# Performance work log

Hardware: AMD Instinct MI355X
Metric: run time of the kernel (lower is better)

The kernel has to match this reference:

```python
import jax, jax.numpy as jnp
import numpy as np

VOCAB, EMB, HID, FF, NCLS = 1000, 32, 32, 16, 7
T, B = 512, 512


def setup_inputs() -> dict:
    key = jax.random.key(0)
    ks = jax.random.split(key, 10)
    s = 1.0 / np.sqrt(HID)
    return {
        "x": jax.random.randint(ks[0], (T, B), 0, VOCAB, dtype=jnp.int64)
        if jax.config.jax_enable_x64 else jax.random.randint(ks[0], (T, B), 0, VOCAB, dtype=jnp.int32),
        "emb": jax.random.normal(ks[1], (VOCAB, EMB), dtype=jnp.float32),
        "W_ih": jax.random.uniform(ks[2], (4 * HID, EMB), minval=-s, maxval=s, dtype=jnp.float32),
        "W_hh": jax.random.uniform(ks[3], (4 * HID, HID), minval=-s, maxval=s, dtype=jnp.float32),
        "b_ih": jax.random.uniform(ks[4], (4 * HID,), minval=-s, maxval=s, dtype=jnp.float32),
        "b_hh": jax.random.uniform(ks[5], (4 * HID,), minval=-s, maxval=s, dtype=jnp.float32),
        "W1": jax.random.uniform(ks[6], (FF, HID), minval=-s, maxval=s, dtype=jnp.float32),
        "b1": jax.random.uniform(ks[7], (FF,), minval=-s, maxval=s, dtype=jnp.float32),
        "W2": jax.random.uniform(ks[8], (NCLS, FF), minval=-s, maxval=s, dtype=jnp.float32),
        "b2": jax.random.uniform(ks[9], (NCLS,), minval=-s, maxval=s, dtype=jnp.float32),
    }


def _lstm(xg, W_hh):
    # xg: (T, B, 4H) precomputed input-to-gate projections (incl. both biases)
    Bn = xg.shape[1]
    h0 = jnp.zeros((Bn, HID), xg.dtype)
    c0 = jnp.zeros((Bn, HID), xg.dtype)

    def step(carry, xg_t):
        h, c = carry
        g = xg_t + h @ W_hh.T  # (B, 4H)
        i, f, gg, o = jnp.split(g, 4, axis=-1)  # PyTorch gate order i,f,g,o
        i = jax.nn.sigmoid(i)
        f = jax.nn.sigmoid(f)
        gg = jnp.tanh(gg)
        o = jax.nn.sigmoid(o)
        c = f * c + i * gg
        h = o * jnp.tanh(c)
        return (h, c), h

    _, hs = jax.lax.scan(step, (h0, c0), xg)
    return hs  # (T, B, H)


def reference(x, emb, W_ih, W_hh, b_ih, b_hh, W1, b1, W2, b2):
    e = emb[x]  # (T, B, EMB) embedding lookup
    xg = jnp.einsum('tbe,ge->tbg', e, W_ih) + b_ih + b_hh  # (T, B, 4H)
    hs = _lstm(xg, W_hh)  # (T, B, H)
    z = jax.nn.relu(jnp.einsum('tbh,fh->tbf', hs, W1) + b1)  # (T, B, FF)
    logits = jnp.einsum('tbf,cf->tbc', z, W2) + b2  # (T, B, NCLS)
    # torch F.softmax with dim=None on a 3D tensor softmaxes over dim 0
    return jax.nn.softmax(logits, axis=0)
```

## Files before the change

### kernel.cpp

```cpp
#include <hip/hip_runtime.h>
#include <math.h>

#define TT    512
#define BB    512
#define HID   32
#define EMB   32
#define FFD   16
#define NCLS  7
#define VOCABN 1000

typedef float v2f __attribute__((ext_vector_type(2)));
typedef float v4f __attribute__((ext_vector_type(4)));

#define NLOG2E  (-1.4426950408889634f)
#define N2LOG2E (-2.8853900817779268f)

__device__ __forceinline__ float rl(float v, int k) {
    return __int_as_float(__builtin_amdgcn_readlane(__float_as_int(v), k));
}
__device__ __forceinline__ float fast_rcp(float x) {
#if defined(__has_builtin)
#if __has_builtin(__builtin_amdgcn_rcpf)
    return __builtin_amdgcn_rcpf(x);
#else
    return 1.0f / x;
#endif
#else
    return 1.0f / x;
#endif
}
__device__ __forceinline__ float sigf(float x) { return fast_rcp(1.0f + __expf(-x)); }
__device__ __forceinline__ float tanh_fast(float x) { return 2.0f * sigf(2.0f * x) - 1.0f; }

__device__ __forceinline__ v2f fma2(v2f a, v2f b, v2f c) {
#if defined(__has_builtin)
#if __has_builtin(__builtin_elementwise_fma)
    return __builtin_elementwise_fma(a, b, c);
#else
    v2f r; r.x = fmaf(a.x, b.x, c.x); r.y = fmaf(a.y, b.y, c.y); return r;
#endif
#else
    v2f r; r.x = fmaf(a.x, b.x, c.x); r.y = fmaf(a.y, b.y, c.y); return r;
#endif
}

__device__ __forceinline__ float xhalf_swap(float v) {
#if defined(__has_builtin)
#if __has_builtin(__builtin_amdgcn_permlane32_swap)
    const unsigned u = __float_as_uint(v);
    auto r = __builtin_amdgcn_permlane32_swap(u, u, false, false);
    return __uint_as_float((r[0] ^ r[1]) ^ u);
#else
    return __shfl_xor(v, 32);
#endif
#else
    return __shfl_xor(v, 32);
#endif
}

__global__ __launch_bounds__(64) void build_xg(
    const float* __restrict__ emb, const float* __restrict__ W_ih,
    const float* __restrict__ b_ih, const float* __restrict__ b_hh,
    float2* __restrict__ tab, int scaled)
{
    const int v = blockIdx.x;
    const int j = threadIdx.x;
    const float* e  = emb + v * EMB;
    const float* w0 = W_ih + j * EMB;
    const float* w1 = W_ih + (j + 64) * EMB;
    float a0 = b_ih[j]      + b_hh[j];
    float a1 = b_ih[j + 64] + b_hh[j + 64];
    #pragma unroll
    for (int k = 0; k < EMB; ++k) {
        const float ek = e[k];
        a0 = fmaf(w0[k], ek, a0);
        a1 = fmaf(w1[k], ek, a1);
    }
    float s0 = 1.0f, s1 = 1.0f;
    if (scaled) { s0 = NLOG2E; s1 = (j < 32) ? N2LOG2E : NLOG2E; }
    tab[v * 64 + j] = make_float2(a0 * s0, a1 * s1);
}

__global__ __launch_bounds__(64)
__attribute__((amdgpu_waves_per_eu(1, 1)))
void lstm_rec(
    const int* __restrict__ x, const float2* __restrict__ tab,
    const float* __restrict__ W_hh, float* __restrict__ hsout)
{
    const int b  = blockIdx.x;
    const int j  = threadIdx.x;
    const int m  = j & 31;
    const bool lo = j < 32;

    __shared__ __align__(16) float sh[8 * HID];

    const float fA = NLOG2E;
    const float fB = lo ? N2LOG2E : NLOG2E;
    const v2f sA2 = {fA, fA};
    const v2f sB2 = {fB, fB};
    const v4f* WA = (const v4f*)(W_hh + j * HID);
    const v4f* WB = (const v4f*)(W_hh + (j + 64) * HID);
    v4f t;
    v2f wpa0,wpa1,wpa2,wpa3,wpa4,wpa5,wpa6,wpa7,wpa8,wpa9,wpa10,wpa11,wpa12,wpa13,wpa14,wpa15;
    v2f wpb0,wpb1,wpb2,wpb3,wpb4,wpb5,wpb6,wpb7,wpb8,wpb9,wpb10,wpb11,wpb12,wpb13,wpb14,wpb15;
    t = WA[0]; wpa0  = t.lo * sA2; wpa1  = t.hi * sA2;
    t = WA[1]; wpa2  = t.lo * sA2; wpa3  = t.hi * sA2;
    t = WA[2]; wpa4  = t.lo * sA2; wpa5  = t.hi * sA2;
    t = WA[3]; wpa6  = t.lo * sA2; wpa7  = t.hi * sA2;
    t = WA[4]; wpa8  = t.lo * sA2; wpa9  = t.hi * sA2;
    t = WA[5]; wpa10 = t.lo * sA2; wpa11 = t.hi * sA2;
    t = WA[6]; wpa12 = t.lo * sA2; wpa13 = t.hi * sA2;
    t = WA[7]; wpa14 = t.lo * sA2; wpa15 = t.hi * sA2;
    t = WB[0]; wpb0  = t.lo * sB2; wpb1  = t.hi * sB2;
    t = WB[1]; wpb2  = t.lo * sB2; wpb3  = t.hi * sB2;
    t = WB[2]; wpb4  = t.lo * sB2; wpb5  = t.hi * sB2;
    t = WB[3]; wpb6  = t.lo * sB2; wpb7  = t.hi * sB2;
    t = WB[4]; wpb8  = t.lo * sB2; wpb9  = t.hi * sB2;
    t = WB[5]; wpb10 = t.lo * sB2; wpb11 = t.hi * sB2;
    t = WB[6]; wpb12 = t.lo * sB2; wpb13 = t.hi * sB2;
    t = WB[7]; wpb14 = t.lo * sB2; wpb15 = t.hi * sB2;

    float h = 0.f, c = 0.f;
    float* hrow0 = hsout + (size_t)b * TT * HID;

    if (lo) sh[7 * HID + m] = 0.0f;

    int xiB[8];
    float2 cxg[8];
    {
        int xi0[8];
        #pragma unroll
        for (int u = 0; u < 8; ++u) xi0[u] = x[u * BB + b];
        #pragma unroll
        for (int u = 0; u < 8; ++u) xiB[u] = x[(8 + u) * BB + b];
        #pragma unroll
        for (int u = 0; u < 8; ++u) cxg[u] = tab[(size_t)xi0[u] * 64 + j];
    }

    for (int t8 = 0; t8 < TT / 8; ++t8) {
        float2 nxg[8];
        #pragma unroll
        for (int u = 0; u < 8; ++u) nxg[u] = tab[(size_t)xiB[u] * 64 + j];
        int xiN[8];
        const int nb2 = (t8 + 2 < TT / 8) ? (t8 + 2) * 8 : 0;
        #pragma unroll
        for (int u = 0; u < 8; ++u) xiN[u] = x[(nb2 + u) * BB + b];

        #pragma unroll
        for (int u = 0; u < 8; ++u) {
            const float* hb = sh + ((u + 7) & 7) * HID;
            const v4f h0 = *(const v4f*)(hb + 0);
            const v4f h1 = *(const v4f*)(hb + 4);
            const v4f h2 = *(const v4f*)(hb + 8);
            const v4f h3 = *(const v4f*)(hb + 12);
            const v4f h4 = *(const v4f*)(hb + 16);
            const v4f h5 = *(const v4f*)(hb + 20);
            const v4f h6 = *(const v4f*)(hb + 24);
            const v4f h7 = *(const v4f*)(hb + 28);

            v2f aP0 = {cxg[u].x, 0.f}, aP1 = {0.f, 0.f};
            v2f aQ0 = {cxg[u].y, 0.f}, aQ1 = {0.f, 0.f};
            aP0 = fma2(wpa0,  h0.lo, aP0);  aP1 = fma2(wpa1,  h0.hi, aP1);
            aQ0 = fma2(wpb0,  h0.lo, aQ0);  aQ1 = fma2(wpb1,  h0.hi, aQ1);
            aP0 = fma2(wpa2,  h1.lo, aP0);  aP1 = fma2(wpa3,  h1.hi, aP1);
            aQ0 = fma2(wpb2,  h1.lo, aQ0);  aQ1 = fma2(wpb3,  h1.hi, aQ1);
            aP0 = fma2(wpa4,  h2.lo, aP0);  aP1 = fma2(wpa5,  h2.hi, aP1);
            aQ0 = fma2(wpb4,  h2.lo, aQ0);  aQ1 = fma2(wpb5,  h2.hi, aQ1);
            aP0 = fma2(wpa6,  h3.lo, aP0);  aP1 = fma2(wpa7,  h3.hi, aP1);
            aQ0 = fma2(wpb6,  h3.lo, aQ0);  aQ1 = fma2(wpb7,  h3.hi, aQ1);
            aP0 = fma2(wpa8,  h4.lo, aP0);  aP1 = fma2(wpa9,  h4.hi, aP1);
            aQ0 = fma2(wpb8,  h4.lo, aQ0);  aQ1 = fma2(wpb9,  h4.hi, aQ1);
            aP0 = fma2(wpa10, h5.lo, aP0);  aP1 = fma2(wpa11, h5.hi, aP1);
            aQ0 = fma2(wpb10, h5.lo, aQ0);  aQ1 = fma2(wpb11, h5.hi, aQ1);
            aP0 = fma2(wpa12, h6.lo, aP0);  aP1 = fma2(wpa13, h6.hi, aP1);
            aQ0 = fma2(wpb12, h6.lo, aQ0);  aQ1 = fma2(wpb13, h6.hi, aQ1);
            aP0 = fma2(wpa14, h7.lo, aP0);  aP1 = fma2(wpa15, h7.hi, aP1);
            aQ0 = fma2(wpb14, h7.lo, aQ0);  aQ1 = fma2(wpb15, h7.hi, aQ1);
            const v2f aP = aP0 + aP1;
            const v2f aQ = aQ0 + aQ1;
            const float accA = aP.x + aP.y;
            const float accB = aQ.x + aQ.y;

            const float actA = fast_rcp(1.0f + __builtin_exp2f(accA));
            const float sgB  = fast_rcp(1.0f + __builtin_exp2f(accB));
            const float actB = lo ? fmaf(2.0f, sgB, -1.0f) : sgB;
            const float oA = xhalf_swap(actA);
            const float oB = xhalf_swap(actB);
            const float gi = lo ? actA : oA;
            const float gf = lo ? oA   : actA;
            const float gg = lo ? actB : oB;
            const float go = lo ? oB   : actB;
            c = fmaf(gf, c, gi * gg);
            const float tc = fmaf(2.0f,
                fast_rcp(1.0f + __builtin_exp2f(c * N2LOG2E)), -1.0f);
            h = go * tc;

            if (lo) sh[u * HID + m] = h;
        }
        const float4 v = *(const float4*)(sh + j * 4);
        *(float4*)(hrow0 + t8 * 8 * HID + j * 4) = v;

        #pragma unroll
        for (int u = 0; u < 8; ++u) { cxg[u] = nxg[u]; xiB[u] = xiN[u]; }
    }
}

__global__ __launch_bounds__(256) void ff_softmax(
    const float* __restrict__ hs,
    const float* __restrict__ W1, const float* __restrict__ b1,
    const float* __restrict__ W2, const float* __restrict__ b2,
    float* __restrict__ out)
{
    const int b    = blockIdx.x;
    const int tid  = threadIdx.x;
    const int lane = tid & 63, wv = tid >> 6;
    const int t0   = tid * 2;

    __shared__ float redM[4][NCLS];
    __shared__ float redS[4][NCLS];

    float4 hv[16];
    const float4* hb = (const float4*)(hs + ((size_t)b * TT + t0) * HID);
    #pragma unroll
    for (int q = 0; q < 16; ++q) hv[q] = hb[q];

    float lg[2][NCLS];
    #pragma unroll
    for (int r = 0; r < 2; ++r) {
        const float* hr = (const float*)(hv + 8 * r);
        float z[FFD];
        #pragma unroll
        for (int f = 0; f < FFD; ++f) {
            float a = b1[f];
            #pragma unroll
            for (int k = 0; k < HID; ++k) a = fmaf(W1[f * HID + k], hr[k], a);
            z[f] = fmaxf(a, 0.f);
        }
        #pragma unroll
        for (int cc = 0; cc < NCLS; ++cc) {
            float a = b2[cc];
            #pragma unroll
            for (int f = 0; f < FFD; ++f) a = fmaf(W2[cc * FFD + f], z[f], a);
            lg[r][cc] = a;
        }
    }

    float M[NCLS], S[NCLS];
    #pragma unroll
    for (int cc = 0; cc < NCLS; ++cc) {
        float mm = fmaxf(lg[0][cc], lg[1][cc]);
        #pragma unroll
        for (int off = 32; off; off >>= 1) mm = fmaxf(mm, __shfl_xor(mm, off));
        if (lane == 0) redM[wv][cc] = mm;
    }
    __syncthreads();
    #pragma unroll
    for (int cc = 0; cc < NCLS; ++cc)
        M[cc] = fmaxf(fmaxf(redM[0][cc], redM[1][cc]), fmaxf(redM[2][cc], redM[3][cc]));

    #pragma unroll
    for (int cc = 0; cc < NCLS; ++cc) {
        float ss = __expf(lg[0][cc] - M[cc]) + __expf(lg[1][cc] - M[cc]);
        #pragma unroll
        for (int off = 32; off; off >>= 1) ss += __shfl_xor(ss, off);
        if (lane == 0) redS[wv][cc] = ss;
    }
    __syncthreads();
    #pragma unroll
    for (int cc = 0; cc < NCLS; ++cc)
        S[cc] = (redS[0][cc] + redS[1][cc]) + (redS[2][cc] + redS[3][cc]);

    #pragma unroll
    for (int r = 0; r < 2; ++r) {
        float* o = out + ((size_t)(t0 + r) * BB + b) * NCLS;
        #pragma unroll
        for (int cc = 0; cc < NCLS; ++cc)
            o[cc] = __expf(lg[r][cc] - M[cc]) * fast_rcp(S[cc]);
    }
}

template <bool TAB>
__global__ __launch_bounds__(64) void lstm_all(
    const int* __restrict__ x, const float* __restrict__ emb,
    const float* __restrict__ W_ih, const float* __restrict__ W_hh,
    const float* __restrict__ b_ih, const float* __restrict__ b_hh,
    const float* __restrict__ W1, const float* __restrict__ b1,
    const float* __restrict__ W2, const float* __restrict__ b2,
    const float2* __restrict__ tab, float* __restrict__ out)
{
    const int b  = blockIdx.x;
    const int j  = threadIdx.x;
    const int m  = j & 31;
    const bool lo = j < 32;
    const int rA = j, rB = j + 64;

    float whhA[HID], whhB[HID];
    #pragma unroll
    for (int k = 0; k < HID; k += 4) {
        float4 a;
        a = *(const float4*)(W_hh + rA * HID + k); whhA[k]=a.x; whhA[k+1]=a.y; whhA[k+2]=a.z; whhA[k+3]=a.w;
        a = *(const float4*)(W_hh + rB * HID + k); whhB[k]=a.x; whhB[k+1]=a.y; whhB[k+2]=a.z; whhB[k+3]=a.w;
    }
    float wihA[HID], wihB[HID];
    float biasA = 0.f, biasB = 0.f;
    if constexpr (!TAB) {
        #pragma unroll
        for (int k = 0; k < HID; k += 4) {
            float4 a;
            a = *(const float4*)(W_ih + rA * HID + k); wihA[k]=a.x; wihA[k+1]=a.y; wihA[k+2]=a.z; wihA[k+3]=a.w;
            a = *(const float4*)(W_ih + rB * HID + k); wihB[k]=a.x; wihB[k+1]=a.y; wihB[k+2]=a.z; wihB[k+3]=a.w;
        }
        biasA = b_ih[rA] + b_hh[rA];
        biasB = b_ih[rB] + b_hh[rB];
    }
    const int f16 = j & 15;
    float w1r[HID];
    #pragma unroll
    for (int k = 0; k < HID; ++k) w1r[k] = W1[f16 * HID + k];
    const int cls = j & 7;
    const int c7  = (cls < NCLS) ? cls : 0;
    float w2r[FFD];
    #pragma unroll
    for (int f = 0; f < FFD; ++f) w2r[f] = W2[c7 * FFD + f];
    const float b1v = b1[f16];
    const float b2v = b2[c7];

    float h = 0.f, c = 0.f;
    float mrun = -3.0e38f, srun = 0.f;

    auto gates = [&](float accA, float accB) {
        const float actA = sigf(accA);
        const float sB   = lo ? 2.0f * accB : accB;
        const float sgB  = sigf(sB);
        const float actB = lo ? 2.0f * sgB - 1.0f : sgB;
        const float oA = __shfl_xor(actA, 32);
        const float oB = __shfl_xor(actB, 32);
        const float gi = lo ? actA : oA;
        const float gf = lo ? oA   : actA;
        const float gg = lo ? actB : oB;
        const float go = lo ? oB   : actB;
        c = fmaf(gf, c, gi * gg);
        h = go * tanh_fast(c);
    };

    auto ff_head = [&](int t_out, const float* hsv) {
        float z0 = b1v, z1 = 0.f;
        #pragma unroll
        for (int k = 0; k < HID; k += 2) {
            z0 = fmaf(w1r[k],     hsv[k],     z0);
            z1 = fmaf(w1r[k + 1], hsv[k + 1], z1);
        }
        const float z = fmaxf(z0 + z1, 0.0f);
        float lgv = b2v;
        #pragma unroll
        for (int f = 0; f < FFD; ++f) lgv = fmaf(w2r[f], rl(z, f), lgv);
        const float mn = fmaxf(mrun, lgv);
        srun = fmaf(srun, __expf(mrun - mn), __expf(lgv - mn));
        mrun = mn;
        if (j < NCLS) out[(t_out * BB + b) * NCLS + j] = lgv;
    };

    int xvn1 = x[1 * BB + b];
    int xvn2 = x[2 * BB + b];
    float2 xg = make_float2(0.f, 0.f);
    float eA = 0.f;
    if constexpr (TAB) xg = tab[(size_t)x[b] * 64 + j];
    else               eA = emb[x[b] * EMB + m];

    if constexpr (TAB) {
        gates(xg.x, xg.y);
    } else {
        float es[EMB];
        #pragma unroll
        for (int k = 0; k < EMB; ++k) es[k] = rl(eA, k);
        float p0 = biasA, p1 = 0.f, q0 = biasB, q1 = 0.f;
        #pragma unroll
        for (int k = 0; k < EMB; k += 2) {
            p0 = fmaf(wihA[k],   es[k],   p0); p1 = fmaf(wihA[k+1], es[k+1], p1);
            q0 = fmaf(wihB[k],   es[k],   q0); q1 = fmaf(wihB[k+1], es[k+1], q1);
        }
        gates(p0 + p1, q0 + q1);
    }
    if constexpr (TAB) xg = tab[(size_t)xvn1 * 64 + j];
    else               eA = emb[xvn1 * EMB + m];
    xvn1 = xvn2;
    xvn2 = x[3 * BB + b];

    for (int t = 1; t < TT; ++t) {
        float2 xg_n = make_float2(0.f, 0.f);
        float  e_n  = 0.f;
        if (t + 1 < TT) {
            if constexpr (TAB) xg_n = tab[(size_t)xvn1 * 64 + j];
            else               e_n  = emb[xvn1 * EMB + m];
        }
        const int xv_n3 = (t + 3 < TT) ? x[(t + 3) * BB + b] : 0;

        float hsv[HID];
        #pragma unroll
        for (int k = 0; k < HID; ++k) hsv[k] = rl(h, k);

        ff_head(t - 1, hsv);

        float p0, p1 = 0.f, q0, q1 = 0.f;
        if constexpr (TAB) { p0 = xg.x; q0 = xg.y; }
        else               { p0 = biasA; q0 = biasB; }
        if constexpr (!TAB) {
            float es[EMB];
            #pragma unroll
            for (int k = 0; k < EMB; ++k) es[k] = rl(eA, k);
            #pragma unroll
            for (int k = 0; k < EMB; k += 2) {
                p0 = fmaf(wihA[k],   es[k],   p0); p1 = fmaf(wihA[k+1], es[k+1], p1);
                q0 = fmaf(wihB[k],   es[k],   q0); q1 = fmaf(wihB[k+1], es[k+1], q1);
            }
        }
        #pragma unroll
        for (int k = 0; k < HID; k += 2) {
            p0 = fmaf(whhA[k],   hsv[k],   p0); p1 = fmaf(whhA[k+1], hsv[k+1], p1);
            q0 = fmaf(whhB[k],   hsv[k],   q0); q1 = fmaf(whhB[k+1], hsv[k+1], q1);
        }
        gates(p0 + p1, q0 + q1);

        xg = xg_n; eA = e_n; xvn1 = xvn2; xvn2 = xv_n3;
    }

    {
        float hsv[HID];
        #pragma unroll
        for (int k = 0; k < HID; ++k) hsv[k] = rl(h, k);
        ff_head(TT - 1, hsv);
    }

    #pragma unroll 1
    for (int cc = 0; cc < NCLS; ++cc) {
        const float mc = rl(mrun, cc);
        const float sc = rl(srun, cc);
        const float ic = 1.0f / sc;
        #pragma unroll
        for (int i = 0; i < TT / 64; ++i) {
            const int t = j + 64 * i;
            const int a = (t * BB + b) * NCLS + cc;
            out[a] = __expf(out[a] - mc) * ic;
        }
    }
}

extern "C" void kernel_launch(void* const* d_in, const int* in_sizes, int n_in,
                              void* d_out, int out_size, void* d_ws, size_t ws_size,
                              hipStream_t stream) {
    const int*   x   = (const int*)  d_in[0];
    const float* emb = (const float*)d_in[1];
    const float* Wih = (const float*)d_in[2];
    const float* Whh = (const float*)d_in[3];
    const float* bih = (const float*)d_in[4];
    const float* bhh = (const float*)d_in[5];
    const float* W1  = (const float*)d_in[6];
    const float* b1  = (const float*)d_in[7];
    const float* W2  = (const float*)d_in[8];
    const float* b2  = (const float*)d_in[9];
    float* out = (float*)d_out;

    const size_t tab_bytes = (size_t)VOCABN * 128 * sizeof(float);
    const size_t hs_off    = 524288;
    const size_t hs_bytes  = (size_t)BB * TT * HID * sizeof(float);
    if (ws_size >= hs_off + hs_bytes) {
        float2* tab = (float2*)d_ws;
        float*  hs  = (float*)((char*)d_ws + hs_off);
        build_xg<<<VOCABN, 64, 0, stream>>>(emb, Wih, bih, bhh, tab, 1);
        lstm_rec<<<BB, 64, 0, stream>>>(x, tab, Whh, hs);
        ff_softmax<<<BB, 256, 0, stream>>>(hs, W1, b1, W2, b2, out);
    } else if (ws_size >= tab_bytes) {
        float2* tab = (float2*)d_ws;
        build_xg<<<VOCABN, 64, 0, stream>>>(emb, Wih, bih, bhh, tab, 0);
        lstm_all<true><<<BB, 64, 0, stream>>>(x, emb, Wih, Whh, bih, bhh,
                                              W1, b1, W2, b2, tab, out);
    } else {
        lstm_all<false><<<BB, 64, 0, stream>>>(x, emb, Wih, Whh, bih, bhh,
                                               W1, b1, W2, b2, nullptr, out);
    }
}
```

Before: 240.1 us.

## Interleave two batch sequences per wavefront in LSTM recurrence

Each 64-thread block now runs the recurrence for two independent batch elements, alternating their timesteps, and launches half as many blocks. The aim is to hide the serial dependency latency (LDS reads, transcendental ops, lane swaps) of one sequence behind the other's independent work. In exchange it uses more registers and halves the block count from 512 to 256. On a 256-CU device this leaves roughly one wave per CU, so per-CU serial work doubles unless the interleaving hides latency well.

```diff
diff --git a/kernel.cpp b/kernel.cpp
--- a/kernel.cpp
+++ b/kernel.cpp
@@ -83,16 +83,18 @@
 
 __global__ __launch_bounds__(64)
 __attribute__((amdgpu_waves_per_eu(1, 1)))
-void lstm_rec(
+void lstm_rec2(
     const int* __restrict__ x, const float2* __restrict__ tab,
     const float* __restrict__ W_hh, float* __restrict__ hsout)
 {
-    const int b  = blockIdx.x;
+    const int b0 = blockIdx.x * 2;
+    const int b1 = b0 + 1;
     const int j  = threadIdx.x;
     const int m  = j & 31;
     const bool lo = j < 32;
 
-    __shared__ __align__(16) float sh[8 * HID];
+    __shared__ __align__(16) float sh0[8 * HID];
+    __shared__ __align__(16) float sh1[8 * HID];
 
     const float fA = NLOG2E;
     const float fB = lo ? N2LOG2E : NLOG2E;
@@ -120,88 +122,110 @@
     t = WB[6]; wpb12 = t.lo * sB2; wpb13 = t.hi * sB2;
     t = WB[7]; wpb14 = t.lo * sB2; wpb15 = t.hi * sB2;
 
-    float h = 0.f, c = 0.f;
-    float* hrow0 = hsout + (size_t)b * TT * HID;
-
-    if (lo) sh[7 * HID + m] = 0.0f;
-
-    int xiB[8];
-    float2 cxg[8];
+    float c0 = 0.f, c1 = 0.f;
+    float* hrow0 = hsout + (size_t)b0 * TT * HID;
+    float* hrow1 = hsout + (size_t)b1 * TT * HID;
+
+    sh0[7 * HID + m] = 0.0f;
+    sh1[7 * HID + m] = 0.0f;
+
+    auto dostep = [&](int u, float* shc, const float2 xgv, float& cc) {
+        const float* hb = shc + ((u + 7) & 7) * HID;
+        const v4f h0 = *(const v4f*)(hb + 0);
+        const v4f h1 = *(const v4f*)(hb + 4);
+        const v4f h2 = *(const v4f*)(hb + 8);
+        const v4f h3 = *(const v4f*)(hb + 12);
+        const v4f h4 = *(const v4f*)(hb + 16);
+        const v4f h5 = *(const v4f*)(hb + 20);
+        const v4f h6 = *(const v4f*)(hb + 24);
+        const v4f h7 = *(const v4f*)(hb + 28);
+
+        v2f aP0 = {xgv.x, 0.f}, aP1 = {0.f, 0.f};
+        v2f aQ0 = {xgv.y, 0.f}, aQ1 = {0.f, 0.f};
+        aP0 = fma2(wpa0,  h0.lo, aP0);  aP1 = fma2(wpa1,  h0.hi, aP1);
+        aQ0 = fma2(wpb0,  h0.lo, aQ0);  aQ1 = fma2(wpb1,  h0.hi, aQ1);
+        aP0 = fma2(wpa2,  h1.lo, aP0);  aP1 = fma2(wpa3,  h1.hi, aP1);
+        aQ0 = fma2(wpb2,  h1.lo, aQ0);  aQ1 = fma2(wpb3,  h1.hi, aQ1);
+        aP0 = fma2(wpa4,  h2.lo, aP0);  aP1 = fma2(wpa5,  h2.hi, aP1);
+        aQ0 = fma2(wpb4,  h2.lo, aQ0);  aQ1 = fma2(wpb5,  h2.hi, aQ1);
+        aP0 = fma2(wpa6,  h3.lo, aP0);  aP1 = fma2(wpa7,  h3.hi, aP1);
+        aQ0 = fma2(wpb6,  h3.lo, aQ0);  aQ1 = fma2(wpb7,  h3.hi, aQ1);
+        aP0 = fma2(wpa8,  h4.lo, aP0);  aP1 = fma2(wpa9,  h4.hi, aP1);
+        aQ0 = fma2(wpb8,  h4.lo, aQ0);  aQ1 = fma2(wpb9,  h4.hi, aQ1);
+        aP0 = fma2(wpa10, h5.lo, aP0);  aP1 = fma2(wpa11, h5.hi, aP1);
+        aQ0 = fma2(wpb10, h5.lo, aQ0);  aQ1 = fma2(wpb11, h5.hi, aQ1);
+        aP0 = fma2(wpa12, h6.lo, aP0);  aP1 = fma2(wpa13, h6.hi, aP1);
+        aQ0 = fma2(wpb12, h6.lo, aQ0);  aQ1 = fma2(wpb13, h6.hi, aQ1);
+        aP0 = fma2(wpa14, h7.lo, aP0);  aP1 = fma2(wpa15, h7.hi, aP1);
+        aQ0 = fma2(wpb14, h7.lo, aQ0);  aQ1 = fma2(wpb15, h7.hi, aQ1);
+        const v2f aP = aP0 + aP1;
+        const v2f aQ = aQ0 + aQ1;
+        const float accA = aP.x + aP.y;
+        const float accB = aQ.x + aQ.y;
+
+        const float actA = fast_rcp(1.0f + __builtin_exp2f(accA));
+        const float sgB  = fast_rcp(1.0f + __builtin_exp2f(accB));
+        const float actB = lo ? fmaf(2.0f, sgB, -1.0f) : sgB;
+        const float oA = xhalf_swap(actA);
+        const float oB = xhalf_swap(actB);
+        const float gi = lo ? actA : oA;
+        const float gf = lo ? oA   : actA;
+        const float gg = lo ? actB : oB;
+        const float go = lo ? oB   : actB;
+        cc = fmaf(gf, cc, gi * gg);
+        const float tc = fmaf(2.0f,
+            fast_rcp(1.0f + __builtin_exp2f(cc * N2LOG2E)), -1.0f);
+        const float hv = go * tc;
+
+        shc[u * HID + m] = hv;
+    };
+
+    int xiB0[8], xiB1[8];
+    float2 cxg0[8], cxg1[8];
     {
-        int xi0[8];
-        #pragma unroll
-        for (int u = 0; u < 8; ++u) xi0[u] = x[u * BB + b];
-        #pragma unroll
-        for (int u = 0; u < 8; ++u) xiB[u] = x[(8 + u) * BB + b];
-        #pragma unroll
-        for (int u = 0; u < 8; ++u) cxg[u] = tab[(size_t)xi0[u] * 64 + j];
+        int xi00[8], xi01[8];
+        #pragma unroll
+        for (int u = 0; u < 8; ++u) { xi00[u] = x[u * BB + b0]; xi01[u] = x[u * BB + b1]; }
+        #pragma unroll
+        for (int u = 0; u < 8; ++u) { xiB0[u] = x[(8 + u) * BB + b0]; xiB1[u] = x[(8 + u) * BB + b1]; }
+        #pragma unroll
+        for (int u = 0; u < 8; ++u) {
+            cxg0[u] = tab[(size_t)xi00[u] * 64 + j];
+            cxg1[u] = tab[(size_t)xi01[u] * 64 + j];
+        }
     }
 
     for (int t8 = 0; t8 < TT / 8; ++t8) {
-        float2 nxg[8];
-        #pragma unroll
-        for (int u = 0; u < 8; ++u) nxg[u] = tab[(size_t)xiB[u] * 64 + j];
-        int xiN[8];
+        float2 nxg0[8], nxg1[8];
+        #pragma unroll
+        for (int u = 0; u < 8; ++u) {
+            nxg0[u] = tab[(size_t)xiB0[u] * 64 + j];
+            nxg1[u] = tab[(size_t)xiB1[u] * 64 + j];
+        }
+        int xiN0[8], xiN1[8];
         const int nb2 = (t8 + 2 < TT / 8) ? (t8 + 2) * 8 : 0;
         #pragma unroll
-        for (int u = 0; u < 8; ++u) xiN[u] = x[(nb2 + u) * BB + b];
-
-        #pragma unroll
         for (int u = 0; u < 8; ++u) {
-            const float* hb = sh + ((u + 7) & 7) * HID;
-            const v4f h0 = *(const v4f*)(hb + 0);
-            const v4f h1 = *(const v4f*)(hb + 4);
-            const v4f h2 = *(const v4f*)(hb + 8);
-            const v4f h3 = *(const v4f*)(hb + 12);
-            const v4f h4 = *(const v4f*)(hb + 16);
-            const v4f h5 = *(const v4f*)(hb + 20);
-            const v4f h6 = *(const v4f*)(hb + 24);
-            const v4f h7 = *(const v4f*)(hb + 28);
-
-            v2f aP0 = {cxg[u].x, 0.f}, aP1 = {0.f, 0.f};
-            v2f aQ0 = {cxg[u].y, 0.f}, aQ1 = {0.f, 0.f};
-            aP0 = fma2(wpa0,  h0.lo, aP0);  aP1 = fma2(wpa1,  h0.hi, aP1);
-            aQ0 = fma2(wpb0,  h0.lo, aQ0);  aQ1 = fma2(wpb1,  h0.hi, aQ1);
-            aP0 = fma2(wpa2,  h1.lo, aP0);  aP1 = fma2(wpa3,  h1.hi, aP1);
-            aQ0 = fma2(wpb2,  h1.lo, aQ0);  aQ1 = fma2(wpb3,  h1.hi, aQ1);
-            aP0 = fma2(wpa4,  h2.lo, aP0);  aP1 = fma2(wpa5,  h2.hi, aP1);
-            aQ0 = fma2(wpb4,  h2.lo, aQ0);  aQ1 = fma2(wpb5,  h2.hi, aQ1);
-            aP0 = fma2(wpa6,  h3.lo, aP0);  aP1 = fma2(wpa7,  h3.hi, aP1);
-            aQ0 = fma2(wpb6,  h3.lo, aQ0);  aQ1 = fma2(wpb7,  h3.hi, aQ1);
-            aP0 = fma2(wpa8,  h4.lo, aP0);  aP1 = fma2(wpa9,  h4.hi, aP1);
-            aQ0 = fma2(wpb8,  h4.lo, aQ0);  aQ1 = fma2(wpb9,  h4.hi, aQ1);
-            aP0 = fma2(wpa10, h5.lo, aP0);  aP1 = fma2(wpa11, h5.hi, aP1);
-            aQ0 = fma2(wpb10, h5.lo, aQ0);  aQ1 = fma2(wpb11, h5.hi, aQ1);
-            aP0 = fma2(wpa12, h6.lo, aP0);  aP1 = fma2(wpa13, h6.hi, aP1);
-            aQ0 = fma2(wpb12, h6.lo, aQ0);  aQ1 = fma2(wpb13, h6.hi, aQ1);
-            aP0 = fma2(wpa14, h7.lo, aP0);  aP1 = fma2(wpa15, h7.hi, aP1);
-            aQ0 = fma2(wpb14, h7.lo, aQ0);  aQ1 = fma2(wpb15, h7.hi, aQ1);
-            const v2f aP = aP0 + aP1;
-            const v2f aQ = aQ0 + aQ1;
-            const float accA = aP.x + aP.y;
-            const float accB = aQ.x + aQ.y;
-
-            const float actA = fast_rcp(1.0f + __builtin_exp2f(accA));
-            const float sgB  = fast_rcp(1.0f + __builtin_exp2f(accB));
-            const float actB = lo ? fmaf(2.0f, sgB, -1.0f) : sgB;
-            const float oA = xhalf_swap(actA);
-            const float oB = xhalf_swap(actB);
-            const float gi = lo ? actA : oA;
-            const float gf = lo ? oA   : actA;
-            const float gg = lo ? actB : oB;
-            const float go = lo ? oB   : actB;
-            c = fmaf(gf, c, gi * gg);
-            const float tc = fmaf(2.0f,
-                fast_rcp(1.0f + __builtin_exp2f(c * N2LOG2E)), -1.0f);
-            h = go * tc;
-
-            if (lo) sh[u * HID + m] = h;
-        }
-        const float4 v = *(const float4*)(sh + j * 4);
-        *(float4*)(hrow0 + t8 * 8 * HID + j * 4) = v;
-
-        #pragma unroll
-        for (int u = 0; u < 8; ++u) { cxg[u] = nxg[u]; xiB[u] = xiN[u]; }
+            xiN0[u] = x[(nb2 + u) * BB + b0];
+            xiN1[u] = x[(nb2 + u) * BB + b1];
+        }
+
+        #pragma unroll
+        for (int u = 0; u < 8; ++u) {
+            dostep(u, sh0, cxg0[u], c0);
+            dostep(u, sh1, cxg1[u], c1);
+        }
+
+        const float4 v0 = *(const float4*)(sh0 + j * 4);
+        *(float4*)(hrow0 + t8 * 8 * HID + j * 4) = v0;
+        const float4 v1 = *(const float4*)(sh1 + j * 4);
+        *(float4*)(hrow1 + t8 * 8 * HID + j * 4) = v1;
+
+        #pragma unroll
+        for (int u = 0; u < 8; ++u) {
+            cxg0[u] = nxg0[u]; xiB0[u] = xiN0[u];
+            cxg1[u] = nxg1[u]; xiB1[u] = xiN1[u];
+        }
     }
 }
 
@@ -467,7 +491,7 @@
         float2* tab = (float2*)d_ws;
         float*  hs  = (float*)((char*)d_ws + hs_off);
         build_xg<<<VOCABN, 64, 0, stream>>>(emb, Wih, bih, bhh, tab, 1);
-        lstm_rec<<<BB, 64, 0, stream>>>(x, tab, Whh, hs);
+        lstm_rec2<<<BB / 2, 64, 0, stream>>>(x, tab, Whh, hs);
         ff_softmax<<<BB, 256, 0, stream>>>(hs, W1, b1, W2, b2, out);
     } else if (ws_size >= tab_bytes) {
         float2* tab = (float2*)d_ws;
```

New measurement: 358.2 us. 49.2% more time.

## Broadcast hidden state via lane swizzles/DPP instead of LDS round-trip

Applied to the files above, without the earlier changes.

Removes the shared-memory buffer used to broadcast h each timestep. Each lane instead gathers all 32 h values through ds_swizzle and DPP xor permutations, and the W_hh weights are loaded in a matching permuted order so each lane's dot product stays correct. The h output is now written straight to global memory per step instead of being staged and stored as float4. This targets the LDS write/read latency on the serial recurrence path, at the cost of many cross-lane ops and narrower, duplicated global stores.

```diff
diff --git a/kernel.cpp b/kernel.cpp
--- a/kernel.cpp
+++ b/kernel.cpp
@@ -57,6 +57,20 @@
     return __shfl_xor(v, 32);
 #endif
 }
+
+#define SWZF(x, imm) __int_as_float(__builtin_amdgcn_ds_swizzle(__float_as_int(x), (imm)))
+#if defined(__has_builtin)
+#if __has_builtin(__builtin_amdgcn_mov_dpp)
+#define XOR1F(x) __int_as_float(__builtin_amdgcn_mov_dpp(__float_as_int(x), 0xB1, 0xF, 0xF, true))
+#define XOR2F(x) __int_as_float(__builtin_amdgcn_mov_dpp(__float_as_int(x), 0x4E, 0xF, 0xF, true))
+#else
+#define XOR1F(x) SWZF(x, 0x041F)
+#define XOR2F(x) SWZF(x, 0x081F)
+#endif
+#else
+#define XOR1F(x) SWZF(x, 0x041F)
+#define XOR2F(x) SWZF(x, 0x081F)
+#endif
 
 __global__ __launch_bounds__(64) void build_xg(
     const float* __restrict__ emb, const float* __restrict__ W_ih,
@@ -92,38 +106,25 @@
     const int m  = j & 31;
     const bool lo = j < 32;
 
-    __shared__ __align__(16) float sh[8 * HID];
-
     const float fA = NLOG2E;
     const float fB = lo ? N2LOG2E : NLOG2E;
     const v2f sA2 = {fA, fA};
     const v2f sB2 = {fB, fB};
-    const v4f* WA = (const v4f*)(W_hh + j * HID);
-    const v4f* WB = (const v4f*)(W_hh + (j + 64) * HID);
-    v4f t;
+    const float* WrA = W_hh + (size_t)j * HID;
+    const float* WrB = W_hh + (size_t)(j + 64) * HID;
     v2f wpa0,wpa1,wpa2,wpa3,wpa4,wpa5,wpa6,wpa7,wpa8,wpa9,wpa10,wpa11,wpa12,wpa13,wpa14,wpa15;
     v2f wpb0,wpb1,wpb2,wpb3,wpb4,wpb5,wpb6,wpb7,wpb8,wpb9,wpb10,wpb11,wpb12,wpb13,wpb14,wpb15;
-    t = WA[0]; wpa0  = t.lo * sA2; wpa1  = t.hi * sA2;
-    t = WA[1]; wpa2  = t.lo * sA2; wpa3  = t.hi * sA2;
-    t = WA[2]; wpa4  = t.lo * sA2; wpa5  = t.hi * sA2;
-    t = WA[3]; wpa6  = t.lo * sA2; wpa7  = t.hi * sA2;
-    t = WA[4]; wpa8  = t.lo * sA2; wpa9  = t.hi * sA2;
-    t = WA[5]; wpa10 = t.lo * sA2; wpa11 = t.hi * sA2;
-    t = WA[6]; wpa12 = t.lo * sA2; wpa13 = t.hi * sA2;
-    t = WA[7]; wpa14 = t.lo * sA2; wpa15 = t.hi * sA2;
-    t = WB[0]; wpb0  = t.lo * sB2; wpb1  = t.hi * sB2;
-    t = WB[1]; wpb2  = t.lo * sB2; wpb3  = t.hi * sB2;
-    t = WB[2]; wpb4  = t.lo * sB2; wpb5  = t.hi * sB2;
-    t = WB[3]; wpb6  = t.lo * sB2; wpb7  = t.hi * sB2;
-    t = WB[4]; wpb8  = t.lo * sB2; wpb9  = t.hi * sB2;
-    t = WB[5]; wpb10 = t.lo * sB2; wpb11 = t.hi * sB2;
-    t = WB[6]; wpb12 = t.lo * sB2; wpb13 = t.hi * sB2;
-    t = WB[7]; wpb14 = t.lo * sB2; wpb15 = t.hi * sB2;
+    #define LDW(t, s0, s1) \
+        wpa##t = (v2f){WrA[m ^ (s0)], WrA[m ^ (s1)]} * sA2; \
+        wpb##t = (v2f){WrB[m ^ (s0)], WrB[m ^ (s1)]} * sB2;
+    LDW(0,  0,  4)  LDW(1,  8, 12)  LDW(2, 16, 20)  LDW(3, 24, 28)
+    LDW(4,  1,  5)  LDW(5,  9, 13)  LDW(6, 17, 21)  LDW(7, 25, 29)
+    LDW(8,  2,  6)  LDW(9, 10, 14)  LDW(10,18, 22)  LDW(11,26, 30)
+    LDW(12, 3,  7)  LDW(13,11, 15)  LDW(14,19, 23)  LDW(15,27, 31)
+    #undef LDW
 
     float h = 0.f, c = 0.f;
     float* hrow0 = hsout + (size_t)b * TT * HID;
-
-    if (lo) sh[7 * HID + m] = 0.0f;
 
     int xiB[8];
     float2 cxg[8];
@@ -148,34 +149,53 @@
 
         #pragma unroll
         for (int u = 0; u < 8; ++u) {
-            const float* hb = sh + ((u + 7) & 7) * HID;
-            const v4f h0 = *(const v4f*)(hb + 0);
-            const v4f h1 = *(const v4f*)(hb + 4);
-            const v4f h2 = *(const v4f*)(hb + 8);
-            const v4f h3 = *(const v4f*)(hb + 12);
-            const v4f h4 = *(const v4f*)(hb + 16);
-            const v4f h5 = *(const v4f*)(hb + 20);
-            const v4f h6 = *(const v4f*)(hb + 24);
-            const v4f h7 = *(const v4f*)(hb + 28);
+            const float u0 = h;
+            const float u1 = SWZF(u0, 0x101F);
+            const float u2 = SWZF(u0, 0x201F);
+            const float u3 = SWZF(u1, 0x201F);
+            const float u4 = SWZF(u0, 0x401F);
+            const float u5 = SWZF(u1, 0x401F);
+            const float u6 = SWZF(u2, 0x401F);
+            const float u7 = SWZF(u3, 0x401F);
+            const float u8  = XOR1F(u0),  u9  = XOR1F(u1);
+            const float u10 = XOR1F(u2),  u11 = XOR1F(u3);
+            const float u12 = XOR1F(u4),  u13 = XOR1F(u5);
+            const float u14 = XOR1F(u6),  u15 = XOR1F(u7);
+            const float u16 = XOR2F(u0),  u17 = XOR2F(u1);
+            const float u18 = XOR2F(u2),  u19 = XOR2F(u3);
+            const float u20 = XOR2F(u4),  u21 = XOR2F(u5);
+            const float u22 = XOR2F(u6),  u23 = XOR2F(u7);
+            const float u24 = XOR2F(u8),  u25 = XOR2F(u9);
+            const float u26 = XOR2F(u10), u27 = XOR2F(u11);
+            const float u28 = XOR2F(u12), u29 = XOR2F(u13);
+            const float u30 = XOR2F(u14), u31 = XOR2F(u15);
+            const v2f hp0  = {u0,  u1},  hp1  = {u2,  u3};
+            const v2f hp2  = {u4,  u5},  hp3  = {u6,  u7};
+            const v2f hp4  = {u8,  u9},  hp5  = {u10, u11};
+            const v2f hp6  = {u12, u13}, hp7  = {u14, u15};
+            const v2f hp8  = {u16, u17}, hp9  = {u18, u19};
+            const v2f hp10 = {u20, u21}, hp11 = {u22, u23};
+            const v2f hp12 = {u24, u25}, hp13 = {u26, u27};
+            const v2f hp14 = {u28, u29}, hp15 = {u30, u31};
 
             v2f aP0 = {cxg[u].x, 0.f}, aP1 = {0.f, 0.f};
             v2f aQ0 = {cxg[u].y, 0.f}, aQ1 = {0.f, 0.f};
-            aP0 = fma2(wpa0,  h0.lo, aP0);  aP1 = fma2(wpa1,  h0.hi, aP1);
-            aQ0 = fma2(wpb0,  h0.lo, aQ0);  aQ1 = fma2(wpb1,  h0.hi, aQ1);
-            aP0 = fma2(wpa2,  h1.lo, aP0);  aP1 = fma2(wpa3,  h1.hi, aP1);
-            aQ0 = fma2(wpb2,  h1.lo, aQ0);  aQ1 = fma2(wpb3,  h1.hi, aQ1);
-            aP0 = fma2(wpa4,  h2.lo, aP0);  aP1 = fma2(wpa5,  h2.hi, aP1);
-            aQ0 = fma2(wpb4,  h2.lo, aQ0);  aQ1 = fma2(wpb5,  h2.hi, aQ1);
-            aP0 = fma2(wpa6,  h3.lo, aP0);  aP1 = fma2(wpa7,  h3.hi, aP1);
-            aQ0 = fma2(wpb6,  h3.lo, aQ0);  aQ1 = fma2(wpb7,  h3.hi, aQ1);
-            aP0 = fma2(wpa8,  h4.lo, aP0);  aP1 = fma2(wpa9,  h4.hi, aP1);
-            aQ0 = fma2(wpb8,  h4.lo, aQ0);  aQ1 = fma2(wpb9,  h4.hi, aQ1);
-            aP0 = fma2(wpa10, h5.lo, aP0);  aP1 = fma2(wpa11, h5.hi, aP1);
-            aQ0 = fma2(wpb10, h5.lo, aQ0);  aQ1 = fma2(wpb11, h5.hi, aQ1);
-            aP0 = fma2(wpa12, h6.lo, aP0);  aP1 = fma2(wpa13, h6.hi, aP1);
-            aQ0 = fma2(wpb12, h6.lo, aQ0);  aQ1 = fma2(wpb13, h6.hi, aQ1);
-            aP0 = fma2(wpa14, h7.lo, aP0);  aP1 = fma2(wpa15, h7.hi, aP1);
-            aQ0 = fma2(wpb14, h7.lo, aQ0);  aQ1 = fma2(wpb15, h7.hi, aQ1);
+            aP0 = fma2(wpa0,  hp0,  aP0);  aQ0 = fma2(wpb0,  hp0,  aQ0);
+            aP1 = fma2(wpa4,  hp4,  aP1);  aQ1 = fma2(wpb4,  hp4,  aQ1);
+            aP0 = fma2(wpa8,  hp8,  aP0);  aQ0 = fma2(wpb8,  hp8,  aQ0);
+            aP1 = fma2(wpa12, hp12, aP1);  aQ1 = fma2(wpb12, hp12, aQ1);
+            aP0 = fma2(wpa1,  hp1,  aP0);  aQ0 = fma2(wpb1,  hp1,  aQ0);
+            aP1 = fma2(wpa2,  hp2,  aP1);  aQ1 = fma2(wpb2,  hp2,  aQ1);
+            aP0 = fma2(wpa5,  hp5,  aP0);  aQ0 = fma2(wpb5,  hp5,  aQ0);
+            aP1 = fma2(wpa6,  hp6,  aP1);  aQ1 = fma2(wpb6,  hp6,  aQ1);
+            aP0 = fma2(wpa9,  hp9,  aP0);  aQ0 = fma2(wpb9,  hp9,  aQ0);
+            aP1 = fma2(wpa10, hp10, aP1);  aQ1 = fma2(wpb10, hp10, aQ1);
+            aP0 = fma2(wpa13, hp13, aP0);  aQ0 = fma2(wpb13, hp13, aQ0);
+            aP1 = fma2(wpa14, hp14, aP1);  aQ1 = fma2(wpb14, hp14, aQ1);
+            aP0 = fma2(wpa3,  hp3,  aP0);  aQ0 = fma2(wpb3,  hp3,  aQ0);
+            aP1 = fma2(wpa7,  hp7,  aP1);  aQ1 = fma2(wpb7,  hp7,  aQ1);
+            aP0 = fma2(wpa11, hp11, aP0);  aQ0 = fma2(wpb11, hp11, aQ0);
+            aP1 = fma2(wpa15, hp15, aP1);  aQ1 = fma2(wpb15, hp15, aQ1);
             const v2f aP = aP0 + aP1;
             const v2f aQ = aQ0 + aQ1;
             const float accA = aP.x + aP.y;
@@ -195,10 +215,8 @@
                 fast_rcp(1.0f + __builtin_exp2f(c * N2LOG2E)), -1.0f);
             h = go * tc;
 
-            if (lo) sh[u * HID + m] = h;
-        }
-        const float4 v = *(const float4*)(sh + j * 4);
-        *(float4*)(hrow0 + t8 * 8 * HID + j * 4) = v;
+            hrow0[(t8 * 8 + u) * HID + m] = h;
+        }
 
         #pragma unroll
         for (int u = 0; u < 8; ++u) { cxg[u] = nxg[u]; xiB[u] = xiN[u]; }
```

After: 287.3 us. +19.7%, slower.

## Fuse feed-forward head and online softmax into the LSTM recurrence kernel

Applied to the files above, without the earlier changes.

Removes the separate ff_softmax kernel and the hidden-state buffer. Each recurrence step now computes the FF head from the previous timestep's h, which is already in registers or LDS, writes raw logits, and keeps a per-class online max and sum for the softmax. A final pass rescales the logits in place. This drops the global round trip of the hidden states but adds per-step work to the latency-bound recurrence critical path.

```diff
diff --git a/kernel.cpp b/kernel.cpp
--- a/kernel.cpp
+++ b/kernel.cpp
@@ -83,9 +83,12 @@
 
 __global__ __launch_bounds__(64)
 __attribute__((amdgpu_waves_per_eu(1, 1)))
-void lstm_rec(
+void lstm_fused(
     const int* __restrict__ x, const float2* __restrict__ tab,
-    const float* __restrict__ W_hh, float* __restrict__ hsout)
+    const float* __restrict__ W_hh,
+    const float* __restrict__ W1, const float* __restrict__ b1,
+    const float* __restrict__ W2, const float* __restrict__ b2,
+    float* __restrict__ out)
 {
     const int b  = blockIdx.x;
     const int j  = threadIdx.x;
@@ -120,8 +123,52 @@
     t = WB[6]; wpb12 = t.lo * sB2; wpb13 = t.hi * sB2;
     t = WB[7]; wpb14 = t.lo * sB2; wpb15 = t.hi * sB2;
 
+    const int f16 = j & 15;
+    const int cls = j & 7;
+    const int c7  = (cls < NCLS) ? cls : 0;
+    v2f w1p0,w1p1,w1p2,w1p3,w1p4,w1p5,w1p6,w1p7,w1p8,w1p9,w1p10,w1p11,w1p12,w1p13,w1p14,w1p15;
+    {
+        const v4f* W1r = (const v4f*)(W1 + f16 * HID);
+        v4f q;
+        q = W1r[0]; w1p0  = q.lo; w1p1  = q.hi;
+        q = W1r[1]; w1p2  = q.lo; w1p3  = q.hi;
+        q = W1r[2]; w1p4  = q.lo; w1p5  = q.hi;
+        q = W1r[3]; w1p6  = q.lo; w1p7  = q.hi;
+        q = W1r[4]; w1p8  = q.lo; w1p9  = q.hi;
+        q = W1r[5]; w1p10 = q.lo; w1p11 = q.hi;
+        q = W1r[6]; w1p12 = q.lo; w1p13 = q.hi;
+        q = W1r[7]; w1p14 = q.lo; w1p15 = q.hi;
+    }
+    float w2r[FFD];
+    #pragma unroll
+    for (int f = 0; f < FFD; ++f) w2r[f] = W2[c7 * FFD + f];
+    const float b1v = b1[f16];
+    const float b2v = b2[c7];
+
     float h = 0.f, c = 0.f;
-    float* hrow0 = hsout + (size_t)b * TT * HID;
+    float mrun = -3.0e38f, srun = 0.f;
+
+    auto ff_head = [&](int t_out, v4f h0, v4f h1, v4f h2, v4f h3,
+                                  v4f h4, v4f h5, v4f h6, v4f h7) {
+        v2f z0 = {b1v, 0.f}, z1 = {0.f, 0.f};
+        z0 = fma2(w1p0,  h0.lo, z0);  z1 = fma2(w1p1,  h0.hi, z1);
+        z0 = fma2(w1p2,  h1.lo, z0);  z1 = fma2(w1p3,  h1.hi, z1);
+        z0 = fma2(w1p4,  h2.lo, z0);  z1 = fma2(w1p5,  h2.hi, z1);
+        z0 = fma2(w1p6,  h3.lo, z0);  z1 = fma2(w1p7,  h3.hi, z1);
+        z0 = fma2(w1p8,  h4.lo, z0);  z1 = fma2(w1p9,  h4.hi, z1);
+        z0 = fma2(w1p10, h5.lo, z0);  z1 = fma2(w1p11, h5.hi, z1);
+        z0 = fma2(w1p12, h6.lo, z0);  z1 = fma2(w1p13, h6.hi, z1);
+        z0 = fma2(w1p14, h7.lo, z0);  z1 = fma2(w1p15, h7.hi, z1);
+        const v2f zs = z0 + z1;
+        const float z = fmaxf(zs.x + zs.y, 0.0f);
+        float lgv = b2v;
+        #pragma unroll
+        for (int f = 0; f < FFD; ++f) lgv = fmaf(w2r[f], rl(z, f), lgv);
+        const float mn = fmaxf(mrun, lgv);
+        srun = fmaf(srun, __expf(mrun - mn), __expf(lgv - mn));
+        mrun = mn;
+        if (j < NCLS) out[((size_t)t_out * BB + b) * NCLS + j] = lgv;
+    };
 
     if (lo) sh[7 * HID + m] = 0.0f;
 
@@ -196,86 +243,39 @@
             h = go * tc;
 
             if (lo) sh[u * HID + m] = h;
-        }
-        const float4 v = *(const float4*)(sh + j * 4);
-        *(float4*)(hrow0 + t8 * 8 * HID + j * 4) = v;
+
+            if (t8 + u > 0)
+                ff_head(t8 * 8 + u - 1, h0, h1, h2, h3, h4, h5, h6, h7);
+        }
 
         #pragma unroll
         for (int u = 0; u < 8; ++u) { cxg[u] = nxg[u]; xiB[u] = xiN[u]; }
     }
-}
-
-__global__ __launch_bounds__(256) void ff_softmax(
-    const float* __restrict__ hs,
-    const float* __restrict__ W1, const float* __restrict__ b1,
-    const float* __restrict__ W2, const float* __restrict__ b2,
-    float* __restrict__ out)
-{
-    const int b    = blockIdx.x;
-    const int tid  = threadIdx.x;
-    const int lane = tid & 63, wv = tid >> 6;
-    const int t0   = tid * 2;
-
-    __shared__ float redM[4][NCLS];
-    __shared__ float redS[4][NCLS];
-
-    float4 hv[16];
-    const float4* hb = (const float4*)(hs + ((size_t)b * TT + t0) * HID);
-    #pragma unroll
-    for (int q = 0; q < 16; ++q) hv[q] = hb[q];
-
-    float lg[2][NCLS];
-    #pragma unroll
-    for (int r = 0; r < 2; ++r) {
-        const float* hr = (const float*)(hv + 8 * r);
-        float z[FFD];
-        #pragma unroll
-        for (int f = 0; f < FFD; ++f) {
-            float a = b1[f];
-            #pragma unroll
-            for (int k = 0; k < HID; ++k) a = fmaf(W1[f * HID + k], hr[k], a);
-            z[f] = fmaxf(a, 0.f);
-        }
-        #pragma unroll
-        for (int cc = 0; cc < NCLS; ++cc) {
-            float a = b2[cc];
-            #pragma unroll
-            for (int f = 0; f < FFD; ++f) a = fmaf(W2[cc * FFD + f], z[f], a);
-            lg[r][cc] = a;
-        }
-    }
-
-    float M[NCLS], S[NCLS];
-    #pragma unroll
+
+    {
+        const float* hb = sh + 7 * HID;
+        const v4f h0 = *(const v4f*)(hb + 0);
+        const v4f h1 = *(const v4f*)(hb + 4);
+        const v4f h2 = *(const v4f*)(hb + 8);
+        const v4f h3 = *(const v4f*)(hb + 12);
+        const v4f h4 = *(const v4f*)(hb + 16);
+        const v4f h5 = *(const v4f*)(hb + 20);
+        const v4f h6 = *(const v4f*)(hb + 24);
+        const v4f h7 = *(const v4f*)(hb + 28);
+        ff_head(TT - 1, h0, h1, h2, h3, h4, h5, h6, h7);
+    }
+
+    #pragma unroll 1
     for (int cc = 0; cc < NCLS; ++cc) {
-        float mm = fmaxf(lg[0][cc], lg[1][cc]);
-        #pragma unroll
-        for (int off = 32; off; off >>= 1) mm = fmaxf(mm, __shfl_xor(mm, off));
-        if (lane == 0) redM[wv][cc] = mm;
-    }
-    __syncthreads();
-    #pragma unroll
-    for (int cc = 0; cc < NCLS; ++cc)
-        M[cc] = fmaxf(fmaxf(redM[0][cc], redM[1][cc]), fmaxf(redM[2][cc], redM[3][cc]));
-
-    #pragma unroll
-    for (int cc = 0; cc < NCLS; ++cc) {
-        float ss = __expf(lg[0][cc] - M[cc]) + __expf(lg[1][cc] - M[cc]);
-        #pragma unroll
-        for (int off = 32; off; off >>= 1) ss += __shfl_xor(ss, off);
-        if (lane == 0) redS[wv][cc] = ss;
-    }
-    __syncthreads();
-    #pragma unroll
-    for (int cc = 0; cc < NCLS; ++cc)
-        S[cc] = (redS[0][cc] + redS[1][cc]) + (redS[2][cc] + redS[3][cc]);
-
-    #pragma unroll
-    for (int r = 0; r < 2; ++r) {
-        float* o = out + ((size_t)(t0 + r) * BB + b) * NCLS;
-        #pragma unroll
-        for (int cc = 0; cc < NCLS; ++cc)
-            o[cc] = __expf(lg[r][cc] - M[cc]) * fast_rcp(S[cc]);
+        const float mc = rl(mrun, cc);
+        const float sc = rl(srun, cc);
+        const float ic = 1.0f / sc;
+        #pragma unroll
+        for (int i = 0; i < TT / 64; ++i) {
+            const int tt = j + 64 * i;
+            const int a = (tt * BB + b) * NCLS + cc;
+            out[a] = __expf(out[a] - mc) * ic;
+        }
     }
 }
 
@@ -461,19 +461,10 @@
     float* out = (float*)d_out;
 
     const size_t tab_bytes = (size_t)VOCABN * 128 * sizeof(float);
-    const size_t hs_off    = 524288;
-    const size_t hs_bytes  = (size_t)BB * TT * HID * sizeof(float);
-    if (ws_size >= hs_off + hs_bytes) {
+    if (ws_size >= tab_bytes) {
         float2* tab = (float2*)d_ws;
-        float*  hs  = (float*)((char*)d_ws + hs_off);
         build_xg<<<VOCABN, 64, 0, stream>>>(emb, Wih, bih, bhh, tab, 1);
-        lstm_rec<<<BB, 64, 0, stream>>>(x, tab, Whh, hs);
-        ff_softmax<<<BB, 256, 0, stream>>>(hs, W1, b1, W2, b2, out);
-    } else if (ws_size >= tab_bytes) {
-        float2* tab = (float2*)d_ws;
-        build_xg<<<VOCABN, 64, 0, stream>>>(emb, Wih, bih, bhh, tab, 0);
-        lstm_all<true><<<BB, 64, 0, stream>>>(x, emb, Wih, Whh, bih, bhh,
-                                              W1, b1, W2, b2, tab, out);
+        lstm_fused<<<BB, 64, 0, stream>>>(x, tab, Whh, W1, b1, W2, b2, out);
     } else {
         lstm_all<false><<<BB, 64, 0, stream>>>(x, emb, Wih, Whh, bih, bhh,
                                                W1, b1, W2, b2, nullptr, out);
```

Result: slower. 375.5 us (+56.4%).
